# Kernel tuning notes

Measured on AMD Instinct MI355X. Metric: run time of the kernel, lower is better.

The kernel has to match this reference:

```python
import jax, jax.numpy as jnp
import numpy as np

B, T, E, S = 16, 2048, 1024, 2000
HID = 150
GI = 3 * E


def _mlp(x, W1, b1, W2, b2, W3, b3):
    # Score module: Linear->ReLU->(Dropout eval=id)->Linear->ReLU->(Dropout)->Linear(->1)
    h = jax.nn.relu(x @ W1 + b1)
    h = jax.nn.relu(h @ W2 + b2)
    return h @ W3 + b3


def setup_inputs() -> dict:
    key = jax.random.key(0)
    ks = jax.random.split(key, 16)
    batch_embeds = jax.random.normal(ks[0], (B, T, E), dtype=jnp.float32)
    starts = jnp.sort(jax.random.randint(ks[1], (B, S), 0, T - 33), axis=-1)
    lengths = jax.random.randint(ks[2], (B, S), 0, 24)
    num_spans = jax.random.randint(ks[3], (B,), 1, S + 1)
    sc = 0.02
    p = lambda k, shape: jax.random.normal(k, shape, dtype=jnp.float32) * sc
    return {
        "batch_embeds": batch_embeds,
        "starts": starts,
        "lengths": lengths,
        "num_spans": num_spans,
        "Wa1": p(ks[4], (E, HID)), "ba1": jnp.zeros((HID,), jnp.float32),
        "Wa2": p(ks[5], (HID, HID)), "ba2": jnp.zeros((HID,), jnp.float32),
        "Wa3": p(ks[6], (HID, 1)), "ba3": jnp.zeros((1,), jnp.float32),
        "Ws1": p(ks[7], (GI, HID)), "bs1": jnp.zeros((HID,), jnp.float32),
        "Ws2": p(ks[8], (HID, HID)), "bs2": jnp.zeros((HID,), jnp.float32),
        "Ws3": p(ks[9], (HID, 1)), "bs3": jnp.zeros((1,), jnp.float32),
    }


def reference(batch_embeds, starts, lengths, num_spans,
              Wa1, ba1, Wa2, ba2, Wa3, ba3,
              Ws1, bs1, Ws2, bs2, Ws3, bs3):
    # attention score per token: [B,T,1]
    attns = _mlp(batch_embeds, Wa1, ba1, Wa2, ba2, Wa3, ba3)
    weighted = batch_embeds * attns  # [B,T,E]
    # prefix sums turn the ragged per-span sum into two gathers per span
    csum = jnp.cumsum(weighted, axis=1)
    csum = jnp.concatenate([jnp.zeros_like(csum[:, :1]), csum], axis=1)  # [B,T+1,E]
    ends = starts + lengths  # inclusive end index, < T
    g_start = jnp.take_along_axis(batch_embeds, starts[..., None], axis=1)  # [B,S,E]
    g_end = jnp.take_along_axis(batch_embeds, ends[..., None], axis=1)      # [B,S,E]
    span_sum = (jnp.take_along_axis(csum, (ends + 1)[..., None], axis=1)
                - jnp.take_along_axis(csum, starts[..., None], axis=1))     # [B,S,E]
    span_emb = jnp.concatenate([g_start, g_end, span_sum], axis=-1)  # [B,S,3E]
    # zero-pad spans beyond each document's span count (matches torch zeros padding)
    mask = (jnp.arange(span_emb.shape[1])[None, :] < num_spans[:, None])[..., None]
    span_emb = jnp.where(mask, span_emb, jnp.zeros((), span_emb.dtype))
    mention_scores = _mlp(span_emb, Ws1, bs1, Ws2, bs2, Ws3, bs3)  # [B,S,1]
    return span_emb, mention_scores
```

## Files before the change

kernel.cpp:

```cpp
#include <hip/hip_runtime.h>
#include <hip/hip_bf16.h>

#define B_   16
#define T_   2048
#define E_   1024
#define S_   2000
#define HID_ 150
#define GI_  3072

typedef __attribute__((ext_vector_type(8))) short short8;
typedef __attribute__((ext_vector_type(4))) float f32x4;

constexpr int NPAD  = 160;
constexpr int LSTR  = 168;
constexpr int MROWS = 64;

__device__ __forceinline__ void gload16(const void* gsrc, void* ldst) {
    __builtin_amdgcn_global_load_lds(
        (const __attribute__((address_space(1))) unsigned int*)gsrc,
        (__attribute__((address_space(3))) unsigned int*)ldst,
        16, 0, 0);
}

__device__ __forceinline__ short8 pack8(float4 a, float4 b) {
    union { __hip_bfloat162 h[4]; short8 s; } u;
    u.h[0] = __float22bfloat162_rn(make_float2(a.x, a.y));
    u.h[1] = __float22bfloat162_rn(make_float2(a.z, a.w));
    u.h[2] = __float22bfloat162_rn(make_float2(b.x, b.y));
    u.h[3] = __float22bfloat162_rn(make_float2(b.z, b.w));
    return u.s;
}

__device__ __forceinline__ short8 pack8v(f32x4 a, f32x4 b) {
    union { __hip_bfloat162 h[4]; short8 s; } u;
    u.h[0] = __float22bfloat162_rn(make_float2(a.x, a.y));
    u.h[1] = __float22bfloat162_rn(make_float2(a.z, a.w));
    u.h[2] = __float22bfloat162_rn(make_float2(b.x, b.y));
    u.h[3] = __float22bfloat162_rn(make_float2(b.z, b.w));
    return u.s;
}

__device__ __forceinline__ void bf16x8_f32(short8 m, f32x4& lo, f32x4& hi) {
    union { short8 s; __hip_bfloat162 h[4]; } u; u.s = m;
    float2 f0 = __bfloat1622float2(u.h[0]);
    float2 f1 = __bfloat1622float2(u.h[1]);
    float2 f2 = __bfloat1622float2(u.h[2]);
    float2 f3 = __bfloat1622float2(u.h[3]);
    lo = (f32x4){f0.x, f0.y, f1.x, f1.y};
    hi = (f32x4){f2.x, f2.y, f3.x, f3.y};
}

__global__ __launch_bounds__(256)
void transpose_all(const float* __restrict__ Wa1, const float* __restrict__ Wa2,
                   const float* __restrict__ Ws1, const float* __restrict__ Ws2,
                   __hip_bfloat16* __restrict__ Wt1a, __hip_bfloat16* __restrict__ Wt2a,
                   __hip_bfloat16* __restrict__ Wt1s, __hip_bfloat16* __restrict__ Wt2s,
                   float* __restrict__ zerobuf)
{
    const int s0 = 160 * 1024, s1 = 160 * 160, s2 = 160 * 3072, s3 = 160 * 160;
    int i = blockIdx.x * 256 + threadIdx.x;
    if (i < s0) {
        int n = i >> 10, k = i & 1023;
        Wt1a[i] = __float2bfloat16(n < HID_ ? Wa1[k * HID_ + n] : 0.f);
    } else if (i < s0 + s1) {
        int j = i - s0, n = j / 160, k = j - n * 160;
        Wt2a[j] = __float2bfloat16((n < HID_ && k < HID_) ? Wa2[k * HID_ + n] : 0.f);
    } else if (i < s0 + s1 + s2) {
        int j = i - s0 - s1, n = j / 3072, k = j - n * 3072;
        Wt1s[j] = __float2bfloat16(n < HID_ ? Ws1[k * HID_ + n] : 0.f);
    } else if (i < s0 + s1 + s2 + s3) {
        int j = i - s0 - s1 - s2, n = j / 160, k = j - n * 160;
        Wt2s[j] = __float2bfloat16((n < HID_ && k < HID_) ? Ws2[k * HID_ + n] : 0.f);
    } else if (i < s0 + s1 + s2 + s3 + 1024) {
        zerobuf[i - s0 - s1 - s2 - s3] = 0.f;
    }
}

template<int K1>
__global__ __launch_bounds__(256, 2)
void mlp_mfma(const float* __restrict__ xin,
              const __hip_bfloat16* __restrict__ Wt1, const float* __restrict__ b1,
              const __hip_bfloat16* __restrict__ Wt2, const float* __restrict__ b2,
              const float* __restrict__ W3, const float* __restrict__ b3,
              float* __restrict__ outp)
{
    constexpr int NC  = K1 / 64;
    constexpr int ACH = 64 * 64 * 4;
    constexpr int BCH = 160 * 64 * 2;
    __shared__ __align__(16) char smem[2 * ACH + 2 * BCH];

    const int tid  = threadIdx.x;
    const int lane = tid & 63;
    const int w    = tid >> 6;
    const int rg   = w >> 1;
    const int cg   = w & 1;
    const int lr   = lane & 15;
    const int hi   = lane >> 4;

    const long long row0 = (long long)blockIdx.x * MROWS;

    auto stageA = [&](int bi, int c) {
        char* dst = smem + bi * ACH;
#pragma unroll
        for (int j = 0; j < 4; ++j) {
            const int row  = (w * 4 + j) * 4 + (lane >> 4);
            const int slot = (lane & 15) ^ (row & 7);
            gload16(xin + (row0 + row) * (long long)K1 + c * 64 + slot * 4,
                    dst + (w * 4 + j) * 1024);
        }
    };
    auto stageB = [&](int bi, int c) {
        char* dst = smem + 2 * ACH + bi * BCH;
#pragma unroll
        for (int j = 0; j < 5; ++j) {
            const int nrow = (w * 5 + j) * 8 + (lane >> 3);
            const int slot = (lane & 7) ^ (nrow & 7);
            gload16(Wt1 + (long long)nrow * K1 + c * 64 + slot * 8,
                    dst + (w * 5 + j) * 1024);
        }
    };

    f32x4 acc[2][5];
#pragma unroll
    for (int rt = 0; rt < 2; ++rt)
#pragma unroll
        for (int nt = 0; nt < 5; ++nt) acc[rt][nt] = (f32x4){0.f, 0.f, 0.f, 0.f};

    stageA(0, 0);
    stageB(0, 0);

    for (int c = 0; c < NC; ++c) {
        __syncthreads();
        if (c + 1 < NC) { stageA((c + 1) & 1, c + 1); stageB((c + 1) & 1, c + 1); }
        const int bi = c & 1;
        const char* sA = smem + bi * ACH;
        const char* sB = smem + 2 * ACH + bi * BCH;
#pragma unroll
        for (int ks = 0; ks < 2; ++ks) {
            short8 bfr[5];
#pragma unroll
            for (int nt = 0; nt < 5; ++nt) {
                const int nrow = cg * 80 + nt * 16 + lr;
                const int slot = (ks * 4 + hi) ^ (nrow & 7);
                bfr[nt] = *(const short8*)(sB + nrow * 128 + slot * 16);
            }
#pragma unroll
            for (int rt = 0; rt < 2; ++rt) {
                const int r = rg * 32 + rt * 16 + lr;
                const int s0i = (ks * 8 + hi * 2) ^ (r & 7);
                const int s1i = (ks * 8 + hi * 2 + 1) ^ (r & 7);
                float4 a0 = *(const float4*)(sA + r * 256 + s0i * 16);
                float4 a1 = *(const float4*)(sA + r * 256 + s1i * 16);
                short8 afr = pack8(a0, a1);
#pragma unroll
                for (int nt = 0; nt < 5; ++nt)
                    acc[rt][nt] = __builtin_amdgcn_mfma_f32_16x16x32_bf16(
                        afr, bfr[nt], acc[rt][nt], 0, 0, 0);
            }
        }
    }
    __syncthreads();

    __hip_bfloat16* hl = (__hip_bfloat16*)smem;

#pragma unroll
    for (int nt = 0; nt < 5; ++nt) {
        const int ch = cg * 80 + nt * 16 + lr;
        const float bb = (ch < HID_) ? b1[ch] : 0.f;
#pragma unroll
        for (int rt = 0; rt < 2; ++rt)
#pragma unroll
            for (int r4 = 0; r4 < 4; ++r4) {
                const int row = rg * 32 + rt * 16 + hi * 4 + r4;
                float h = acc[rt][nt][r4] + bb;
                hl[row * LSTR + ch] = __float2bfloat16(h > 0.f ? h : 0.f);
            }
    }
    __syncthreads();

    f32x4 acc2[2][5];
#pragma unroll
    for (int rt = 0; rt < 2; ++rt)
#pragma unroll
        for (int nt = 0; nt < 5; ++nt) acc2[rt][nt] = (f32x4){0.f, 0.f, 0.f, 0.f};

#pragma unroll
    for (int ks = 0; ks < 5; ++ks) {
        const int k0 = ks * 32 + hi * 8;
        short8 bfr[5];
#pragma unroll
        for (int nt = 0; nt < 5; ++nt)
            bfr[nt] = *(const short8*)(Wt2 + (cg * 80 + nt * 16 + lr) * NPAD + k0);
#pragma unroll
        for (int rt = 0; rt < 2; ++rt) {
            short8 afr = *(const short8*)&hl[(rg * 32 + rt * 16 + lr) * LSTR + k0];
#pragma unroll
            for (int nt = 0; nt < 5; ++nt)
                acc2[rt][nt] = __builtin_amdgcn_mfma_f32_16x16x32_bf16(
                    afr, bfr[nt], acc2[rt][nt], 0, 0, 0);
        }
    }
    __syncthreads();

#pragma unroll
    for (int nt = 0; nt < 5; ++nt) {
        const int ch = cg * 80 + nt * 16 + lr;
        const float bb = (ch < HID_) ? b2[ch] : 0.f;
#pragma unroll
        for (int rt = 0; rt < 2; ++rt)
#pragma unroll
            for (int r4 = 0; r4 < 4; ++r4) {
                const int row = rg * 32 + rt * 16 + hi * 4 + r4;
                float h = acc2[rt][nt][r4] + bb;
                hl[row * LSTR + ch] = __float2bfloat16(h > 0.f ? h : 0.f);
            }
    }
    __syncthreads();

    {
        const int row = tid >> 2, quad = tid & 3;
        const int kb = quad * 38;
        const int ke = (kb + 38 > HID_) ? HID_ : kb + 38;
        float s = 0.f;
        for (int k = kb; k < ke; ++k)
            s += __bfloat162float(hl[row * LSTR + k]) * W3[k];
        s += __shfl_xor(s, 1);
        s += __shfl_xor(s, 2);
        if (quad == 0) outp[row0 + row] = s + b3[0];
    }
}

__global__ __launch_bounds__(256)
void wsum_tiles(const float* __restrict__ x, const float* __restrict__ attn,
                float* __restrict__ P)
{
    const int b = blockIdx.x >> 5, tile = blockIdx.x & 31, q = threadIdx.x;
    const float* xb = x + ((long long)b * T_ + tile * 64) * E_ + q * 4;
    const float* ab = attn + b * T_ + tile * 64;
    f32x4 a0 = (f32x4){0.f, 0.f, 0.f, 0.f}, a1 = a0;
#pragma unroll 8
    for (int t = 0; t < 64; t += 2) {
        a0 += ab[t]     * *(const f32x4*)(xb + (long long)t * E_);
        a1 += ab[t + 1] * *(const f32x4*)(xb + (long long)(t + 1) * E_);
    }
    *(f32x4*)(P + ((long long)(b * 32 + tile)) * E_ + q * 4) = a0 + a1;
}

__global__ __launch_bounds__(256)
void wcumsum(const float* __restrict__ x, const float* __restrict__ attn,
             const float* __restrict__ P, __hip_bfloat16* __restrict__ csum)
{
    const int b = blockIdx.x >> 5, tile = blockIdx.x & 31, q = threadIdx.x;
    f32x4 pfx = (f32x4){0.f, 0.f, 0.f, 0.f};
    for (int tau = 0; tau < tile; ++tau)
        pfx += *(const f32x4*)(P + ((long long)(b * 32 + tau)) * E_ + q * 4);
    const float* xb = x + ((long long)b * T_ + tile * 64) * E_ + q * 4;
    __hip_bfloat16* cb = csum + ((long long)b * T_ + tile * 64) * E_ + q * 4;
    const float* ab = attn + b * T_ + tile * 64;
    f32x4 acc = pfx;
#pragma unroll 4
    for (int t = 0; t < 64; ++t) {
        acc += ab[t] * *(const f32x4*)(xb + (long long)t * E_);
        union { __hip_bfloat162 h[2]; uint2 u; } cv;
        cv.h[0] = __float22bfloat162_rn(make_float2(acc.x, acc.y));
        cv.h[1] = __float22bfloat162_rn(make_float2(acc.z, acc.w));
        *(uint2*)(cb + (long long)t * E_) = cv.u;
    }
}

__global__ __launch_bounds__(512, 4)
void span_score(const float* __restrict__ x, const __hip_bfloat16* __restrict__ csum,
                const float* __restrict__ zrow,
                const int* __restrict__ starts, const int* __restrict__ lengths,
                const int* __restrict__ nspans,
                const __hip_bfloat16* __restrict__ Wt1, const float* __restrict__ b1,
                const __hip_bfloat16* __restrict__ Wt2, const float* __restrict__ b2,
                const float* __restrict__ W3, const float* __restrict__ b3,
                float* __restrict__ spanout, float* __restrict__ scoreout)
{
    __shared__ __align__(16) char smem[58112];
    int* stL = (int*)(smem + 57344);
    int* enL = (int*)(smem + 57600);
    int* bL  = (int*)(smem + 57856);

    const int tid  = threadIdx.x;
    const int lane = tid & 63;
    const int w    = tid >> 6;
    const int rg   = w >> 1;
    const int cg   = w & 1;
    const int lr   = lane & 15;
    const int hi   = lane >> 4;

    int bid = blockIdx.x;
    {
        const int qq = 500 / 8, rr = 500 % 8;
        const int xcd = bid % 8, i = bid / 8;
        bid = (xcd < rr ? xcd * (qq + 1) : rr * (qq + 1) + (xcd - rr) * qq) + i;
    }
    const int span0 = bid * 64;

    if (tid < 64) {
        const int sp = span0 + tid;
        const int b  = sp / S_;
        const int s  = sp - b * S_;
        const bool val = s < nspans[b];
        const int st = val ? starts[sp] : 0;
        stL[tid] = st;
        enL[tid] = val ? (st + lengths[sp]) : -1;
        bL[tid]  = b;
    }
    __syncthreads();

    const int r    = tid >> 3;
    const int q    = tid & 7;
    const int st_r = stL[r];
    const int en_r = enL[r];
    const bool valid = en_r >= st_r;
    const long long sp_r = span0 + r;
    const float* xb = x + (long long)bL[r] * T_ * E_;
    const __hip_bfloat16* cbh = csum + (long long)bL[r] * T_ * E_;
    const __hip_bfloat16* zrh = (const __hip_bfloat16*)zrow;

    const float* px_st = valid ? xb + (long long)st_r * E_ : zrow;
    const float* px_en = valid ? xb + (long long)en_r * E_ : zrow;
    const __hip_bfloat16* pc_en = valid ? cbh + (long long)en_r * E_ : zrh;
    const __hip_bfloat16* pc_st = (valid && st_r > 0) ? cbh + (long long)(st_r - 1) * E_ : zrh;

    auto ldreg = [&](int c, f32x4& l0, f32x4& l1, short8& m0, short8& m1) {
        const int off = (c & 15) * 64 + q * 8;
        if (c < 32) {
            const float* s1 = (c < 16) ? px_st : px_en;
            l0 = *(const f32x4*)(s1 + off);
            l1 = *(const f32x4*)(s1 + off + 4);
        } else {
            m0 = *(const short8*)(pc_en + off);
            m1 = *(const short8*)(pc_st + off);
        }
    };
    auto emit = [&](int bi, int c, f32x4 l0, f32x4 l1, short8 m0, short8 m1) {
        f32x4 v0, v1;
        if (c < 32) { v0 = l0; v1 = l1; }
        else {
            f32x4 e0, e1, s0, s1;
            bf16x8_f32(m0, e0, e1);
            bf16x8_f32(m1, s0, s1);
            v0 = e0 - s0; v1 = e1 - s1;
        }
        float* orow = spanout + sp_r * (3 * E_) + c * 64 + q * 8;
        __builtin_nontemporal_store(v0, (f32x4*)orow);
        __builtin_nontemporal_store(v1, (f32x4*)(orow + 4));
        *(short8*)(smem + bi * 8192 + r * 128 + ((q ^ (r & 7)) * 16)) = pack8v(v0, v1);
    };
    auto stageB = [&](int bi, int c) {
        char* dst = smem + 16384 + bi * 20480;
#pragma unroll
        for (int j = 0; j < 3; ++j) {
            const int idx = w * 3 + j;
            if (idx < 20) {
                const int nrow = idx * 8 + (lane >> 3);
                const int slot = (lane & 7) ^ (nrow & 7);
                gload16(Wt1 + (long long)nrow * GI_ + c * 64 + slot * 8,
                        dst + idx * 1024);
            }
        }
    };

    f32x4 acc[5];
#pragma unroll
    for (int nt = 0; nt < 5; ++nt) acc[nt] = (f32x4){0.f, 0.f, 0.f, 0.f};

    f32x4 pA0, pA1;  short8 mA0, mA1;
    f32x4 pB0, pB1;  short8 mB0, mB1;

    stageB(0, 0);
    asm volatile("" ::: "memory");
    ldreg(0, pA0, pA1, mA0, mA1);
    emit(0, 0, pA0, pA1, mA0, mA1);
    ldreg(1, pB0, pB1, mB0, mB1);

    auto phase = [&](int c, f32x4& u0, f32x4& u1, short8& um0, short8& um1,
                     f32x4& f0, f32x4& f1, short8& fm0, short8& fm1) {
        asm volatile("s_waitcnt vmcnt(4) lgkmcnt(0)" ::: "memory");
        __builtin_amdgcn_s_barrier();
        const int bi = c & 1;
        if (c + 1 < 48) {
            stageB(bi ^ 1, c + 1);
            asm volatile("" ::: "memory");
            if (c + 2 < 48) ldreg(c + 2, f0, f1, fm0, fm1);
            asm volatile("" ::: "memory");
            emit(bi ^ 1, c + 1, u0, u1, um0, um1);
        }
        const char* sAc = smem + bi * 8192;
        const char* sBc = smem + 16384 + bi * 20480;
#pragma unroll
        for (int ks = 0; ks < 2; ++ks) {
            short8 bfr[5];
#pragma unroll
            for (int nt = 0; nt < 5; ++nt) {
                const int nrow = cg * 80 + nt * 16 + lr;
                const int slot = (ks * 4 + hi) ^ (nrow & 7);
                bfr[nt] = *(const short8*)(sBc + nrow * 128 + slot * 16);
            }
            const int r2 = rg * 16 + lr;
            const int sl = (ks * 4 + hi) ^ (r2 & 7);
            short8 afr = *(const short8*)(sAc + r2 * 128 + sl * 16);
#pragma unroll
            for (int nt = 0; nt < 5; ++nt)
                acc[nt] = __builtin_amdgcn_mfma_f32_16x16x32_bf16(
                    afr, bfr[nt], acc[nt], 0, 0, 0);
        }
    };

    for (int cc = 0; cc < 48; cc += 2) {
        phase(cc,     pB0, pB1, mB0, mB1, pA0, pA1, mA0, mA1);
        phase(cc + 1, pA0, pA1, mA0, mA1, pB0, pB1, mB0, mB1);
    }
    asm volatile("s_waitcnt lgkmcnt(0)" ::: "memory");
    __builtin_amdgcn_s_barrier();

    __hip_bfloat16* hl = (__hip_bfloat16*)smem;

#pragma unroll
    for (int nt = 0; nt < 5; ++nt) {
        const int ch = cg * 80 + nt * 16 + lr;
        const float bb = (ch < HID_) ? b1[ch] : 0.f;
#pragma unroll
        for (int r4 = 0; r4 < 4; ++r4) {
            const int row = rg * 16 + hi * 4 + r4;
            float h = acc[nt][r4] + bb;
            hl[row * LSTR + ch] = __float2bfloat16(h > 0.f ? h : 0.f);
        }
    }
    __syncthreads();

    f32x4 acc2[5];
#pragma unroll
    for (int nt = 0; nt < 5; ++nt) acc2[nt] = (f32x4){0.f, 0.f, 0.f, 0.f};

#pragma unroll
    for (int ks = 0; ks < 5; ++ks) {
        const int k0 = ks * 32 + hi * 8;
        short8 bfr[5];
#pragma unroll
        for (int nt = 0; nt < 5; ++nt)
            bfr[nt] = *(const short8*)(Wt2 + (cg * 80 + nt * 16 + lr) * NPAD + k0);
        short8 afr = *(const short8*)&hl[(rg * 16 + lr) * LSTR + k0];
#pragma unroll
        for (int nt = 0; nt < 5; ++nt)
            acc2[nt] = __builtin_amdgcn_mfma_f32_16x16x32_bf16(
                afr, bfr[nt], acc2[nt], 0, 0, 0);
    }
    __syncthreads();

#pragma unroll
    for (int nt = 0; nt < 5; ++nt) {
        const int ch = cg * 80 + nt * 16 + lr;
        const float bb = (ch < HID_) ? b2[ch] : 0.f;
#pragma unroll
        for (int r4 = 0; r4 < 4; ++r4) {
            const int row = rg * 16 + hi * 4 + r4;
            float h = acc2[nt][r4] + bb;
            hl[row * LSTR + ch] = __float2bfloat16(h > 0.f ? h : 0.f);
        }
    }
    __syncthreads();

    {
        const int row = tid >> 3, oct = tid & 7;
        const int kb = oct * 19;
        const int ke = (kb + 19 > HID_) ? HID_ : kb + 19;
        float s = 0.f;
        for (int k = kb; k < ke; ++k)
            s += __bfloat162float(hl[row * LSTR + k]) * W3[k];
        s += __shfl_xor(s, 1);
        s += __shfl_xor(s, 2);
        s += __shfl_xor(s, 4);
        if (oct == 0) scoreout[span0 + row] = s + b3[0];
    }
}

extern "C" void kernel_launch(void* const* d_in, const int* in_sizes, int n_in,
                              void* d_out, int out_size, void* d_ws, size_t ws_size,
                              hipStream_t stream) {
    const float* x       = (const float*)d_in[0];
    const int*   starts  = (const int*)d_in[1];
    const int*   lengths = (const int*)d_in[2];
    const int*   nspans  = (const int*)d_in[3];
    const float* Wa1 = (const float*)d_in[4];
    const float* ba1 = (const float*)d_in[5];
    const float* Wa2 = (const float*)d_in[6];
    const float* ba2 = (const float*)d_in[7];
    const float* Wa3 = (const float*)d_in[8];
    const float* ba3 = (const float*)d_in[9];
    const float* Ws1 = (const float*)d_in[10];
    const float* bs1 = (const float*)d_in[11];
    const float* Ws2 = (const float*)d_in[12];
    const float* bs2 = (const float*)d_in[13];
    const float* Ws3 = (const float*)d_in[14];
    const float* bs3 = (const float*)d_in[15];

    float* out        = (float*)d_out;
    float* out_scores = out + (long long)B_ * S_ * 3 * E_;

    char* ws = (char*)d_ws;
    float*          attn    = (float*)ws;
    __hip_bfloat16* Wt1a    = (__hip_bfloat16*)(ws + 131072);
    __hip_bfloat16* Wt2a    = (__hip_bfloat16*)(ws + 458752);
    __hip_bfloat16* Wt1s    = (__hip_bfloat16*)(ws + 509952);
    __hip_bfloat16* Wt2s    = (__hip_bfloat16*)(ws + 1492992);
    float*          zerobuf = (float*)(ws + 1544192);
    float*          Ptile   = (float*)(ws + 2097152);
    __hip_bfloat16* csum    = (__hip_bfloat16*)(ws + 4194304);

    transpose_all<<<2765, 256, 0, stream>>>(Wa1, Wa2, Ws1, Ws2,
                                            Wt1a, Wt2a, Wt1s, Wt2s, zerobuf);

    mlp_mfma<E_><<<(B_ * T_) / MROWS, 256, 0, stream>>>
        (x, Wt1a, ba1, Wt2a, ba2, Wa3, ba3, attn);

    wsum_tiles<<<B_ * 32, 256, 0, stream>>>(x, attn, Ptile);
    wcumsum   <<<B_ * 32, 256, 0, stream>>>(x, attn, Ptile, csum);

    span_score<<<500, 512, 0, stream>>>
        (x, csum, zerobuf, starts, lengths, nspans,
         Wt1s, bs1, Wt2s, bs2, Ws3, bs3, out, out_scores);
}
```

Before: 254.9 us.

## Materialize bf16 shadow of embeddings to halve downstream gather and scan reads

wsum_tiles now also writes a bf16 copy of the input embeddings. wcumsum and span_score then read that copy instead of the fp32 tensor, which halves the bytes read for the cumulative-sum pass and for the start/end gathers. span_score's load and emit path is unified onto bf16 short8 loads. Its pipelined loop is restructured with an explicit final phase and a separate MFMA tail. In exchange there is an extra 64 MB write pass, and the start/end columns of the output are now bf16-rounded rather than exact fp32 copies, which could exceed tolerance.

```diff
diff --git a/kernel.cpp b/kernel.cpp
--- a/kernel.cpp
+++ b/kernel.cpp
@@ -48,6 +48,20 @@
     float2 f3 = __bfloat1622float2(u.h[3]);
     lo = (f32x4){f0.x, f0.y, f1.x, f1.y};
     hi = (f32x4){f2.x, f2.y, f3.x, f3.y};
+}
+
+__device__ __forceinline__ f32x4 bf16x4_f32u(uint2 v) {
+    union { uint2 u2; __hip_bfloat162 h[2]; } c; c.u2 = v;
+    float2 f0 = __bfloat1622float2(c.h[0]);
+    float2 f1 = __bfloat1622float2(c.h[1]);
+    return (f32x4){f0.x, f0.y, f1.x, f1.y};
+}
+
+__device__ __forceinline__ uint2 f32x4_bf16u(f32x4 v) {
+    union { __hip_bfloat162 h[2]; uint2 u; } cv;
+    cv.h[0] = __float22bfloat162_rn(make_float2(v.x, v.y));
+    cv.h[1] = __float22bfloat162_rn(make_float2(v.z, v.w));
+    return cv.u;
 }
 
 __global__ __launch_bounds__(256)
@@ -232,44 +246,48 @@
 
 __global__ __launch_bounds__(256)
 void wsum_tiles(const float* __restrict__ x, const float* __restrict__ attn,
-                float* __restrict__ P)
+                float* __restrict__ P, __hip_bfloat16* __restrict__ shadow)
 {
     const int b = blockIdx.x >> 5, tile = blockIdx.x & 31, q = threadIdx.x;
     const float* xb = x + ((long long)b * T_ + tile * 64) * E_ + q * 4;
+    __hip_bfloat16* sb = shadow + ((long long)b * T_ + tile * 64) * E_ + q * 4;
     const float* ab = attn + b * T_ + tile * 64;
     f32x4 a0 = (f32x4){0.f, 0.f, 0.f, 0.f}, a1 = a0;
-#pragma unroll 8
+#pragma unroll 4
     for (int t = 0; t < 64; t += 2) {
-        a0 += ab[t]     * *(const f32x4*)(xb + (long long)t * E_);
-        a1 += ab[t + 1] * *(const f32x4*)(xb + (long long)(t + 1) * E_);
+        f32x4 v0 = *(const f32x4*)(xb + (long long)t * E_);
+        f32x4 v1 = *(const f32x4*)(xb + (long long)(t + 1) * E_);
+        a0 += ab[t] * v0;
+        a1 += ab[t + 1] * v1;
+        *(uint2*)(sb + (long long)t * E_)       = f32x4_bf16u(v0);
+        *(uint2*)(sb + (long long)(t + 1) * E_) = f32x4_bf16u(v1);
     }
     *(f32x4*)(P + ((long long)(b * 32 + tile)) * E_ + q * 4) = a0 + a1;
 }
 
 __global__ __launch_bounds__(256)
-void wcumsum(const float* __restrict__ x, const float* __restrict__ attn,
+void wcumsum(const __hip_bfloat16* __restrict__ shadow, const float* __restrict__ attn,
              const float* __restrict__ P, __hip_bfloat16* __restrict__ csum)
 {
     const int b = blockIdx.x >> 5, tile = blockIdx.x & 31, q = threadIdx.x;
     f32x4 pfx = (f32x4){0.f, 0.f, 0.f, 0.f};
     for (int tau = 0; tau < tile; ++tau)
         pfx += *(const f32x4*)(P + ((long long)(b * 32 + tau)) * E_ + q * 4);
-    const float* xb = x + ((long long)b * T_ + tile * 64) * E_ + q * 4;
+    const __hip_bfloat16* sb = shadow + ((long long)b * T_ + tile * 64) * E_ + q * 4;
     __hip_bfloat16* cb = csum + ((long long)b * T_ + tile * 64) * E_ + q * 4;
     const float* ab = attn + b * T_ + tile * 64;
     f32x4 acc = pfx;
 #pragma unroll 4
     for (int t = 0; t < 64; ++t) {
-        acc += ab[t] * *(const f32x4*)(xb + (long long)t * E_);
-        union { __hip_bfloat162 h[2]; uint2 u; } cv;
-        cv.h[0] = __float22bfloat162_rn(make_float2(acc.x, acc.y));
-        cv.h[1] = __float22bfloat162_rn(make_float2(acc.z, acc.w));
-        *(uint2*)(cb + (long long)t * E_) = cv.u;
+        f32x4 v = bf16x4_f32u(*(const uint2*)(sb + (long long)t * E_));
+        acc += ab[t] * v;
+        *(uint2*)(cb + (long long)t * E_) = f32x4_bf16u(acc);
     }
 }
 
 __global__ __launch_bounds__(512, 4)
-void span_score(const float* __restrict__ x, const __hip_bfloat16* __restrict__ csum,
+void span_score(const __hip_bfloat16* __restrict__ shadow,
+                const __hip_bfloat16* __restrict__ csum,
                 const float* __restrict__ zrow,
                 const int* __restrict__ starts, const int* __restrict__ lengths,
                 const int* __restrict__ nspans,
@@ -317,35 +335,27 @@
     const int en_r = enL[r];
     const bool valid = en_r >= st_r;
     const long long sp_r = span0 + r;
-    const float* xb = x + (long long)bL[r] * T_ * E_;
-    const __hip_bfloat16* cbh = csum + (long long)bL[r] * T_ * E_;
+    const __hip_bfloat16* shb = shadow + (long long)bL[r] * T_ * E_;
+    const __hip_bfloat16* cbh = csum   + (long long)bL[r] * T_ * E_;
     const __hip_bfloat16* zrh = (const __hip_bfloat16*)zrow;
 
-    const float* px_st = valid ? xb + (long long)st_r * E_ : zrow;
-    const float* px_en = valid ? xb + (long long)en_r * E_ : zrow;
+    const __hip_bfloat16* ps_st = valid ? shb + (long long)st_r * E_ : zrh;
+    const __hip_bfloat16* ps_en = valid ? shb + (long long)en_r * E_ : zrh;
     const __hip_bfloat16* pc_en = valid ? cbh + (long long)en_r * E_ : zrh;
     const __hip_bfloat16* pc_st = (valid && st_r > 0) ? cbh + (long long)(st_r - 1) * E_ : zrh;
 
-    auto ldreg = [&](int c, f32x4& l0, f32x4& l1, short8& m0, short8& m1) {
+    auto ldreg = [&](int c, short8& m0, short8& m1) {
+        const __hip_bfloat16* s1 = (c < 16) ? ps_st : ((c < 32) ? ps_en : pc_en);
+        const __hip_bfloat16* s2 = (c < 32) ? zrh : pc_st;
         const int off = (c & 15) * 64 + q * 8;
-        if (c < 32) {
-            const float* s1 = (c < 16) ? px_st : px_en;
-            l0 = *(const f32x4*)(s1 + off);
-            l1 = *(const f32x4*)(s1 + off + 4);
-        } else {
-            m0 = *(const short8*)(pc_en + off);
-            m1 = *(const short8*)(pc_st + off);
-        }
-    };
-    auto emit = [&](int bi, int c, f32x4 l0, f32x4 l1, short8 m0, short8 m1) {
-        f32x4 v0, v1;
-        if (c < 32) { v0 = l0; v1 = l1; }
-        else {
-            f32x4 e0, e1, s0, s1;
-            bf16x8_f32(m0, e0, e1);
-            bf16x8_f32(m1, s0, s1);
-            v0 = e0 - s0; v1 = e1 - s1;
-        }
+        m0 = *(const short8*)(s1 + off);
+        m1 = *(const short8*)(s2 + off);
+    };
+    auto emit = [&](int bi, int c, short8 m0, short8 m1) {
+        f32x4 e0, e1, s0, s1v;
+        bf16x8_f32(m0, e0, e1);
+        bf16x8_f32(m1, s0, s1v);
+        f32x4 v0 = e0 - s0, v1 = e1 - s1v;
         float* orow = spanout + sp_r * (3 * E_) + c * 64 + q * 8;
         __builtin_nontemporal_store(v0, (f32x4*)orow);
         __builtin_nontemporal_store(v1, (f32x4*)(orow + 4));
@@ -369,27 +379,16 @@
 #pragma unroll
     for (int nt = 0; nt < 5; ++nt) acc[nt] = (f32x4){0.f, 0.f, 0.f, 0.f};
 
-    f32x4 pA0, pA1;  short8 mA0, mA1;
-    f32x4 pB0, pB1;  short8 mB0, mB1;
+    short8 mA0, mA1;
+    short8 mB0, mB1;
 
     stageB(0, 0);
     asm volatile("" ::: "memory");
-    ldreg(0, pA0, pA1, mA0, mA1);
-    emit(0, 0, pA0, pA1, mA0, mA1);
-    ldreg(1, pB0, pB1, mB0, mB1);
-
-    auto phase = [&](int c, f32x4& u0, f32x4& u1, short8& um0, short8& um1,
-                     f32x4& f0, f32x4& f1, short8& fm0, short8& fm1) {
-        asm volatile("s_waitcnt vmcnt(4) lgkmcnt(0)" ::: "memory");
-        __builtin_amdgcn_s_barrier();
-        const int bi = c & 1;
-        if (c + 1 < 48) {
-            stageB(bi ^ 1, c + 1);
-            asm volatile("" ::: "memory");
-            if (c + 2 < 48) ldreg(c + 2, f0, f1, fm0, fm1);
-            asm volatile("" ::: "memory");
-            emit(bi ^ 1, c + 1, u0, u1, um0, um1);
-        }
+    ldreg(0, mA0, mA1);
+    emit(0, 0, mA0, mA1);
+    ldreg(1, mB0, mB1);
+
+    auto mfma_block = [&](int bi) {
         const char* sAc = smem + bi * 8192;
         const char* sBc = smem + 16384 + bi * 20480;
 #pragma unroll
@@ -411,10 +410,29 @@
         }
     };
 
-    for (int cc = 0; cc < 48; cc += 2) {
-        phase(cc,     pB0, pB1, mB0, mB1, pA0, pA1, mA0, mA1);
-        phase(cc + 1, pA0, pA1, mA0, mA1, pB0, pB1, mB0, mB1);
-    }
+    auto phase = [&](int c, short8& u0, short8& u1, short8& f0, short8& f1) {
+        asm volatile("s_waitcnt vmcnt(4) lgkmcnt(0)" ::: "memory");
+        __builtin_amdgcn_s_barrier();
+        const int bi = c & 1;
+        if (c + 1 < 48) {
+            stageB(bi ^ 1, c + 1);
+            asm volatile("" ::: "memory");
+            if (c + 2 < 48) ldreg(c + 2, f0, f1);
+            asm volatile("" ::: "memory");
+            emit(bi ^ 1, c + 1, u0, u1);
+        }
+        mfma_block(bi);
+    };
+
+    for (int cc = 0; cc < 46; cc += 2) {
+        phase(cc,     mB0, mB1, mA0, mA1);
+        phase(cc + 1, mA0, mA1, mB0, mB1);
+    }
+    phase(46, mB0, mB1, mA0, mA1);
+    asm volatile("s_waitcnt vmcnt(2) lgkmcnt(0)" ::: "memory");
+    __builtin_amdgcn_s_barrier();
+    mfma_block(1);
+
     asm volatile("s_waitcnt lgkmcnt(0)" ::: "memory");
     __builtin_amdgcn_s_barrier();
 
@@ -511,6 +529,7 @@
     float*          zerobuf = (float*)(ws + 1544192);
     float*          Ptile   = (float*)(ws + 2097152);
     __hip_bfloat16* csum    = (__hip_bfloat16*)(ws + 4194304);
+    __hip_bfloat16* shadow  = (__hip_bfloat16*)(ws + 71303168);
 
     transpose_all<<<2765, 256, 0, stream>>>(Wa1, Wa2, Ws1, Ws2,
                                             Wt1a, Wt2a, Wt1s, Wt2s, zerobuf);
@@ -518,10 +537,10 @@
     mlp_mfma<E_><<<(B_ * T_) / MROWS, 256, 0, stream>>>
         (x, Wt1a, ba1, Wt2a, ba2, Wa3, ba3, attn);
 
-    wsum_tiles<<<B_ * 32, 256, 0, stream>>>(x, attn, Ptile);
-    wcumsum   <<<B_ * 32, 256, 0, stream>>>(x, attn, Ptile, csum);
+    wsum_tiles<<<B_ * 32, 256, 0, stream>>>(x, attn, Ptile, shadow);
+    wcumsum   <<<B_ * 32, 256, 0, stream>>>(shadow, attn, Ptile, csum);
 
     span_score<<<500, 512, 0, stream>>>
-        (x, csum, zerobuf, starts, lengths, nspans,
+        (shadow, csum, zerobuf, starts, lengths, nspans,
          Wt1s, bs1, Wt2s, bs2, Ws3, bs3, out, out_scores);
 }
```

Result: slower. 262.9 us (+3.1%).
